# Optimization experiments

Hardware: AMD Instinct MI355X
Metric: run time of the kernel (lower is better)

## Reference

```python
import jax, jax.numpy as jnp
import numpy as np

NEG_SLOPE = 0.2  # PyG GATConv default leaky_relu slope

N_NODES = 50000
N_EDGES = 800000
IN_DIM = 128
HID = 32
HEADS = 4


def setup_inputs() -> dict:
    key = jax.random.key(0)
    ks = jax.random.split(key, 12)
    x = jax.random.normal(ks[0], (N_NODES, IN_DIM), dtype=jnp.float32)
    edge_index = jax.random.randint(ks[1], (2, N_EDGES), 0, N_NODES, dtype=jnp.int64)
    s1 = 1.0 / np.sqrt(IN_DIM)
    s2 = 1.0 / np.sqrt(HID * HEADS)
    return {
        "x": x,
        "edge_index": edge_index,
        # layer 1: GATConv(IN_DIM -> HID, heads=HEADS, concat=True)
        "W1": jax.random.normal(ks[2], (IN_DIM, HEADS * HID), dtype=jnp.float32) * s1,
        "a_src1": jax.random.normal(ks[3], (HEADS, HID), dtype=jnp.float32) * s1,
        "a_dst1": jax.random.normal(ks[4], (HEADS, HID), dtype=jnp.float32) * s1,
        "b1": jnp.zeros((HEADS * HID,), dtype=jnp.float32),
        # head: GATConv(HEADS*HID -> 1, heads=1, concat=False)
        "W2": jax.random.normal(ks[5], (HEADS * HID, 1), dtype=jnp.float32) * s2,
        "a_src2": jax.random.normal(ks[6], (1, 1), dtype=jnp.float32) * s2,
        "a_dst2": jax.random.normal(ks[7], (1, 1), dtype=jnp.float32) * s2,
        "b2": jnp.zeros((1,), dtype=jnp.float32),
    }


def gat_conv(x, src, dst, W, a_src, a_dst, b, heads, out_ch, concat, n_nodes):
    # linear transform -> [N, H, C]
    h = (x @ W).reshape(n_nodes, heads, out_ch)
    # per-node attention halves -> [N, H]
    alpha_s = jnp.einsum('nhc,hc->nh', h, a_src)
    alpha_d = jnp.einsum('nhc,hc->nh', h, a_dst)
    # per-edge logits (gather), leaky relu -> [E, H]
    e = jax.nn.leaky_relu(alpha_s[src] + alpha_d[dst], NEG_SLOPE)
    # segment softmax over destination neighborhoods
    m = jax.ops.segment_max(e, dst, num_segments=n_nodes)  # [N, H]
    m = jnp.where(jnp.isfinite(m), m, 0.0)
    ex = jnp.exp(e - m[dst])
    denom = jax.ops.segment_sum(ex, dst, num_segments=n_nodes)  # [N, H]
    alpha = ex / (denom[dst] + 1e-16)  # [E, H]
    # weighted scatter-aggregate of source messages
    msg = h[src] * alpha[:, :, None]  # [E, H, C]
    out = jax.ops.segment_sum(msg, dst, num_segments=n_nodes)  # [N, H, C]
    out = out.reshape(n_nodes, heads * out_ch) if concat else out.mean(axis=1)
    return out + b


def reference(x, edge_index, W1, a_src1, a_dst1, b1, W2, a_src2, a_dst2, b2):
    n = x.shape[0]
    # PyG GATConv adds self-loops by default
    loops = jnp.arange(n, dtype=edge_index.dtype)
    src = jnp.concatenate([edge_index[0], loops])
    dst = jnp.concatenate([edge_index[1], loops])
    h = gat_conv(x, src, dst, W1, a_src1, a_dst1, b1, HEADS, HID, True, n)
    h = jax.nn.elu(h)  # dropout inactive in eval mode
    out = gat_conv(h, src, dst, W2, a_src2, a_dst2, b2, 1, 1, False, n)
    return out.squeeze(-1)  # [N]
```

## Files before the change

kernel.cpp:

```cpp
#include <hip/hip_runtime.h>
#include <hip/hip_bf16.h>
#include <hip/hip_fp16.h>

#define N_NODES 50000
#define N_EDGES 800000
#define E_TOT   850000
#define GBLK 32
#define GEMM_BLOCKS 1563
#define NR 196
#define EPB 4096
#define BIN_BLOCKS 208
#define WT_BLOCKS 32
#define SEGCAP 8192

typedef _Float16 half8 __attribute__((ext_vector_type(8)));
typedef float f32x16 __attribute__((ext_vector_type(16)));

__global__ __launch_bounds__(512) void bin_kernel(const int* __restrict__ ei,
                                                  int* __restrict__ rangeCursor,
                                                  unsigned* __restrict__ gseg,
                                                  const float* __restrict__ W1,
                                                  _Float16* __restrict__ Wt) {
    __shared__ int cnt[NR];
    __shared__ int gbase[NR];
    const int tid = threadIdx.x;

    if (blockIdx.x >= BIN_BLOCKS) {
        int k = (blockIdx.x - BIN_BLOCKS) * 4 + (tid >> 7);
        int c = tid & 127;
        Wt[c * 128 + k] = (_Float16)W1[k * 128 + c];
        return;
    }

    for (int i = tid; i < NR; i += 512) cnt[i] = 0;
    __syncthreads();

    int e0 = blockIdx.x * EPB + tid * 8;
    bool valid = (e0 < E_TOT);
    int src[8], dst[8], rg[8], rk[8];
    if (valid) {
        if (e0 < N_EDGES) {
            int4 a = *(const int4*)(ei + e0);
            int4 b = *(const int4*)(ei + e0 + 4);
            int4 c = *(const int4*)(ei + N_EDGES + e0);
            int4 d = *(const int4*)(ei + N_EDGES + e0 + 4);
            src[0]=a.x; src[1]=a.y; src[2]=a.z; src[3]=a.w;
            src[4]=b.x; src[5]=b.y; src[6]=b.z; src[7]=b.w;
            dst[0]=c.x; dst[1]=c.y; dst[2]=c.z; dst[3]=c.w;
            dst[4]=d.x; dst[5]=d.y; dst[6]=d.z; dst[7]=d.w;
        } else {
#pragma unroll
            for (int k = 0; k < 8; k++) { src[k] = dst[k] = e0 + k - N_EDGES; }
        }
#pragma unroll
        for (int k = 0; k < 8; k++) {
            rg[k] = dst[k] >> 8;
            rk[k] = atomicAdd(&cnt[rg[k]], 1);
        }
    }
    __syncthreads();
    for (int i = tid; i < NR; i += 512) {
        int c = cnt[i];
        gbase[i] = c ? atomicAdd(&rangeCursor[i], c) : 0;
    }
    __syncthreads();
    if (valid) {
#pragma unroll
        for (int k = 0; k < 8; k++) {
            int pos = gbase[rg[k]] + rk[k];
            if (pos < SEGCAP)
                gseg[(size_t)rg[k] * SEGCAP + pos] =
                    ((unsigned)(dst[k] & 255) << 17) | (unsigned)src[k];
        }
    }
}

__global__ __launch_bounds__(512) void fatgf_kernel(const int* __restrict__ rangeCursor,
                                                    const unsigned* __restrict__ gseg,
                                                    int* __restrict__ offs,
                                                    int* __restrict__ bucket,
                                                    const float* __restrict__ x,
                                                    const _Float16* __restrict__ Wt,
                                                    const float* __restrict__ asrc1,
                                                    const float* __restrict__ adst1,
                                                    __half* __restrict__ h1,
                                                    float* __restrict__ as1,
                                                    float* __restrict__ ad1) {
    __shared__ __align__(16) char smem[(1024 + SEGCAP) * 4];
    const int tid = threadIdx.x;

    if (blockIdx.x < NR) {
        int* rsc  = (int*)smem;
        int* cnt  = rsc + 256;
        int* csc  = cnt + 256;
        int* cur  = csc + 256;
        int* lbuf = cur + 256;
        const int r = blockIdx.x;

        if (tid < 256) rsc[tid] = (tid < NR) ? min(rangeCursor[tid], SEGCAP) : 0;
        __syncthreads();
        for (int d = 1; d < 256; d <<= 1) {
            int u = (tid < 256 && tid >= d) ? rsc[tid - d] : 0;
            __syncthreads();
            if (tid < 256) rsc[tid] += u;
            __syncthreads();
        }
        const int n = min(rangeCursor[r], SEGCAP);
        const int rbase = rsc[r] - n;
        const unsigned* __restrict__ seg = gseg + (size_t)r * SEGCAP;

        if (tid < 256) cnt[tid] = 0;
        __syncthreads();
        for (int i = tid; i < n; i += 512)
            atomicAdd(&cnt[seg[i] >> 17], 1);
        __syncthreads();
        if (tid < 256) csc[tid] = cnt[tid];
        __syncthreads();
        for (int d = 1; d < 256; d <<= 1) {
            int u = (tid < 256 && tid >= d) ? csc[tid - d] : 0;
            __syncthreads();
            if (tid < 256) csc[tid] += u;
            __syncthreads();
        }
        if (tid < 256) {
            int lofs = csc[tid] - cnt[tid];
            cur[tid] = lofs;
            int node = r * 256 + tid;
            if (node < N_NODES) offs[node] = rbase + lofs;
        }
        if (r == NR - 1 && tid == 0) offs[N_NODES] = rbase + n;
        __syncthreads();
        for (int i = tid; i < n; i += 512) {
            unsigned en = seg[i];
            int p = atomicAdd(&cur[en >> 17], 1);
            lbuf[p] = (int)(en & 0x1FFFFu);
        }
        __syncthreads();
        for (int i = tid; i < n; i += 512)
            bucket[rbase + i] = lbuf[i];
        return;
    }

    if (tid >= 256) return;

    _Float16* hl = (_Float16*)smem;
    const int l    = tid & 63;
    const int w    = tid >> 6;
    const int g    = l >> 5;
    const int cl   = l & 31;
    const int col  = 32 * w + cl;
    const int base = (blockIdx.x - NR) * GBLK;
    int r = base + cl;
    int rc = (r < N_NODES) ? r : 0;

    const half8* wt8 = (const half8*)(Wt + col * 128);
    half8 bf0 = wt8[0 + g], bf1 = wt8[2 + g], bf2 = wt8[4 + g], bf3 = wt8[6 + g];
    half8 bf4 = wt8[8 + g], bf5 = wt8[10 + g], bf6 = wt8[12 + g], bf7 = wt8[14 + g];

    const float* xr = x + (size_t)rc * 128 + 8 * g;
    f32x16 acc = {};
#define GAT_MFMA_STEP(S, BF)                                                  \
    {                                                                         \
        float4 u0 = *(const float4*)(xr + 16 * S);                            \
        float4 u1 = *(const float4*)(xr + 16 * S + 4);                        \
        half8 af;                                                             \
        af[0] = (_Float16)u0.x; af[1] = (_Float16)u0.y;                       \
        af[2] = (_Float16)u0.z; af[3] = (_Float16)u0.w;                       \
        af[4] = (_Float16)u1.x; af[5] = (_Float16)u1.y;                       \
        af[6] = (_Float16)u1.z; af[7] = (_Float16)u1.w;                       \
        acc = __builtin_amdgcn_mfma_f32_32x32x16_f16(af, BF, acc, 0, 0, 0);   \
    }
    GAT_MFMA_STEP(0, bf0) GAT_MFMA_STEP(1, bf1) GAT_MFMA_STEP(2, bf2)
    GAT_MFMA_STEP(3, bf3) GAT_MFMA_STEP(4, bf4) GAT_MFMA_STEP(5, bf5)
    GAT_MFMA_STEP(6, bf6) GAT_MFMA_STEP(7, bf7)
#undef GAT_MFMA_STEP

#pragma unroll
    for (int j = 0; j < 16; j++) {
        int nl = (j & 3) + 8 * (j >> 2) + 4 * g;
        hl[nl * 136 + col] = (_Float16)acc[j];
    }
    __syncthreads();

    {
        int nl = tid >> 3, c8 = tid & 7;
        int node = base + nl;
        if (node < N_NODES) {
            float4 v0 = *(const float4*)(hl + nl * 136 + c8 * 16);
            float4 v1 = *(const float4*)(hl + nl * 136 + c8 * 16 + 8);
            float4* dst = (float4*)(h1 + (size_t)node * 128 + c8 * 16);
            dst[0] = v0;
            dst[1] = v1;
        }
    }
    {
        int nh = tid >> 1, which = tid & 1;
        int nl = nh & 31, head = nh >> 5;
        int node = base + nl;
        if (node < N_NODES) {
            const float* av = (which ? adst1 : asrc1) + head * 32;
            const _Float16* hp = hl + nl * 136 + head * 32;
            float s = 0.f;
#pragma unroll
            for (int j = 0; j < 32; j++)
                s += (float)hp[j] * av[j];
            (which ? ad1 : as1)[node * 4 + head] = s;
        }
    }
}

__global__ __launch_bounds__(256) void agg1_kernel(const __half* __restrict__ h1,
                                                   const float* __restrict__ as1,
                                                   const float* __restrict__ ad1,
                                                   const int* __restrict__ offs,
                                                   const int* __restrict__ bucket,
                                                   const float* __restrict__ b1,
                                                   const float* __restrict__ W2,
                                                   float* __restrict__ h2s) {
    __shared__ int   sbuf[4][64];
    __shared__ float exbuf[4][64][4];

    int w = threadIdx.x >> 6, l = threadIdx.x & 63;
    int node = blockIdx.x * 4 + w;
    if (node >= N_NODES) return;
    int sub = l & 15;
    int ep  = l >> 4;
    int head = sub >> 2;
    int a = offs[node];
    int deg = offs[node + 1] - a;
    float4 adv = *(const float4*)(ad1 + (size_t)node * 4);

    float c[8];
#pragma unroll
    for (int k = 0; k < 8; k++) c[k] = 0.f;
    float sx = 0.f;

    for (int base = 0; base < deg; base += 64) {
        int cd = min(deg - base, 64);
        {
            bool v = l < cd;
            int s = bucket[a + base + (v ? l : 0)];
            sbuf[w][l] = s;
            float4 asv = *(const float4*)(as1 + (size_t)s * 4);
            float e0 = asv.x + adv.x, e1 = asv.y + adv.y;
            float e2 = asv.z + adv.z, e3 = asv.w + adv.w;
            e0 = fmaxf(e0, 0.2f * e0);
            e1 = fmaxf(e1, 0.2f * e1);
            e2 = fmaxf(e2, 0.2f * e2);
            e3 = fmaxf(e3, 0.2f * e3);
            float4 exv;
            exv.x = v ? __expf(e0) : 0.f;
            exv.y = v ? __expf(e1) : 0.f;
            exv.z = v ? __expf(e2) : 0.f;
            exv.w = v ? __expf(e3) : 0.f;
            *(float4*)&exbuf[w][l][0] = exv;
        }
        __builtin_amdgcn_wave_barrier();
        for (int g = 0; g < cd; g += 4) {
            int j = g + ep;
            bool v2 = j < cd;
            int jj = v2 ? j : 0;
            int s = sbuf[w][jj];
            float ex = exbuf[w][jj][head];
            if (!v2) ex = 0.f;
            float4 hv = *(const float4*)(h1 + (size_t)s * 128 + sub * 8);
            const __half2* hh = (const __half2*)&hv;
            float2 f0 = __half22float2(hh[0]);
            float2 f1 = __half22float2(hh[1]);
            float2 f2 = __half22float2(hh[2]);
            float2 f3 = __half22float2(hh[3]);
            sx += ex;
            c[0] += ex * f0.x; c[1] += ex * f0.y;
            c[2] += ex * f1.x; c[3] += ex * f1.y;
            c[4] += ex * f2.x; c[5] += ex * f2.y;
            c[6] += ex * f3.x; c[7] += ex * f3.y;
        }
        __builtin_amdgcn_wave_barrier();
    }

#pragma unroll
    for (int k = 0; k < 8; k++) {
        c[k] += __shfl_xor(c[k], 16, 64);
        c[k] += __shfl_xor(c[k], 32, 64);
    }
    sx += __shfl_xor(sx, 16, 64);
    sx += __shfl_xor(sx, 32, 64);

    float r = 1.f / (sx + 1e-16f);
    float4 blo = ((const float4*)b1)[sub * 2];
    float4 bhi = ((const float4*)b1)[sub * 2 + 1];
    float4 wlo = ((const float4*)W2)[sub * 2];
    float4 whi = ((const float4*)W2)[sub * 2 + 1];
    float ob[8] = {blo.x, blo.y, blo.z, blo.w, bhi.x, bhi.y, bhi.z, bhi.w};
    float ow[8] = {wlo.x, wlo.y, wlo.z, wlo.w, whi.x, whi.y, whi.z, whi.w};
    float p = 0.f;
#pragma unroll
    for (int k = 0; k < 8; k++) {
        float o = c[k] * r + ob[k];
        float el = (o > 0.f) ? o : (__expf(o) - 1.f);
        p += el * ow[k];
    }
    p += __shfl_xor(p, 1, 64);
    p += __shfl_xor(p, 2, 64);
    p += __shfl_xor(p, 4, 64);
    p += __shfl_xor(p, 8, 64);
    if (l == 0) h2s[node] = p;
}

__global__ __launch_bounds__(256) void agg2_kernel(const float* __restrict__ h2s,
                                                   const int* __restrict__ offs,
                                                   const int* __restrict__ bucket,
                                                   const float* __restrict__ asrc2,
                                                   const float* __restrict__ adst2,
                                                   const float* __restrict__ b2,
                                                   float* __restrict__ out) {
    int w = threadIdx.x >> 6, l = threadIdx.x & 63;
    int node = blockIdx.x * 4 + w;
    if (node >= N_NODES) return;
    float asc = asrc2[0], adc = adst2[0], bias = b2[0];
    float adn = h2s[node] * adc;
    int a = offs[node], b = offs[node + 1];
    float sx = 0.f, sw = 0.f;
    for (int i = a + l; i < b; i += 64) {
        float hs = h2s[bucket[i]];
        float e = hs * asc + adn;
        e = fmaxf(e, 0.2f * e);
        float ex = __expf(e);
        sx += ex;
        sw += ex * hs;
    }
#pragma unroll
    for (int o = 32; o > 0; o >>= 1) {
        sx += __shfl_xor(sx, o, 64);
        sw += __shfl_xor(sw, o, 64);
    }
    if (l == 0) out[node] = sw / (sx + 1e-16f) + bias;
}


extern "C" void kernel_launch(void* const* d_in, const int* in_sizes, int n_in,
                              void* d_out, int out_size, void* d_ws, size_t ws_size,
                              hipStream_t stream) {
    const float* x     = (const float*)d_in[0];
    const int*   ei    = (const int*)d_in[1];
    const float* W1    = (const float*)d_in[2];
    const float* asrc1 = (const float*)d_in[3];
    const float* adst1 = (const float*)d_in[4];
    const float* b1    = (const float*)d_in[5];
    const float* W2    = (const float*)d_in[6];
    const float* asrc2 = (const float*)d_in[7];
    const float* adst2 = (const float*)d_in[8];
    const float* b2    = (const float*)d_in[9];
    float* out = (float*)d_out;

    char* ws = (char*)d_ws;
    size_t o = 0;
    auto alloc = [&](size_t bytes) -> void* {
        void* p = ws + o;
        o += (bytes + 255) & ~(size_t)255;
        return p;
    };
    int* offs    = (int*)alloc((size_t)(N_NODES + 1) * 4);
    int* bucket  = (int*)alloc((size_t)E_TOT * 4);
    __half* h1   = (__half*)alloc((size_t)N_NODES * 128 * 2);
    float* as1   = (float*)alloc((size_t)N_NODES * 4 * 4);
    float* ad1   = (float*)alloc((size_t)N_NODES * 4 * 4);
    float* h2s   = (float*)alloc((size_t)N_NODES * 4);
    int* rangeCursor = (int*)alloc((size_t)NR * 4);
    unsigned* gseg   = (unsigned*)alloc((size_t)NR * SEGCAP * 4);
    _Float16* Wt     = (_Float16*)alloc((size_t)128 * 128 * 2);

    hipMemsetAsync(rangeCursor, 0, (size_t)NR * 4, stream);

    bin_kernel<<<BIN_BLOCKS + WT_BLOCKS, 512, 0, stream>>>(ei, rangeCursor, gseg, W1, Wt);

    fatgf_kernel<<<NR + GEMM_BLOCKS, 512, 0, stream>>>(
        rangeCursor, gseg, offs, bucket,
        x, Wt, asrc1, adst1, h1, as1, ad1);

    agg1_kernel<<<(N_NODES + 3) / 4, 256, 0, stream>>>(
        h1, as1, ad1, offs, bucket, b1, W2, h2s);

    agg2_kernel<<<(N_NODES + 3) / 4, 256, 0, stream>>>(
        h2s, offs, bucket, asrc2, adst2, b2, out);
}
```

Before: 95.21 us.

## Stage x tile in LDS as fp16 and double GEMM rows per block

The node-feature GEMM block now handles 64 rows instead of 32 and uses all 512 threads instead of idling half of them. The x tile is loaded with coalesced float4 reads, converted to fp16 once, and stored in a padded LDS buffer; each MFMA wave then reads its A operand from LDS. The attention-score epilogue is remapped to the 64-row tile. This aims to improve global load coalescing and cut block count and per-block overhead, at the cost of more LDS per block and an extra barrier.

Measured after the change: 110.5 us. +16.1%, slower.

```diff
diff --git a/kernel.cpp b/kernel.cpp
--- a/kernel.cpp
+++ b/kernel.cpp
@@ -5,13 +5,14 @@
 #define N_NODES 50000
 #define N_EDGES 800000
 #define E_TOT   850000
-#define GBLK 32
-#define GEMM_BLOCKS 1563
+#define GBLK 64
+#define GEMM_BLOCKS 782
 #define NR 196
 #define EPB 4096
 #define BIN_BLOCKS 208
 #define WT_BLOCKS 32
 #define SEGCAP 8192
+#define XS_STRIDE 134
 
 typedef _Float16 half8 __attribute__((ext_vector_type(8)));
 typedef float f32x16 __attribute__((ext_vector_type(16)));
@@ -141,44 +142,54 @@
         return;
     }
 
-    if (tid >= 256) return;
-
-    _Float16* hl = (_Float16*)smem;
-    const int l    = tid & 63;
-    const int w    = tid >> 6;
-    const int g    = l >> 5;
-    const int cl   = l & 31;
-    const int col  = 32 * w + cl;
+    _Float16* xs = (_Float16*)smem;
+    _Float16* hl = (_Float16*)(smem + 64 * XS_STRIDE * 2);
     const int base = (blockIdx.x - NR) * GBLK;
-    int r = base + cl;
-    int rc = (r < N_NODES) ? r : 0;
-
-    const half8* wt8 = (const half8*)(Wt + col * 128);
-    half8 bf0 = wt8[0 + g], bf1 = wt8[2 + g], bf2 = wt8[4 + g], bf3 = wt8[6 + g];
-    half8 bf4 = wt8[8 + g], bf5 = wt8[10 + g], bf6 = wt8[12 + g], bf7 = wt8[14 + g];
-
-    const float* xr = x + (size_t)rc * 128 + 8 * g;
-    f32x16 acc = {};
-#define GAT_MFMA_STEP(S, BF)                                                  \
-    {                                                                         \
-        float4 u0 = *(const float4*)(xr + 16 * S);                            \
-        float4 u1 = *(const float4*)(xr + 16 * S + 4);                        \
-        half8 af;                                                             \
-        af[0] = (_Float16)u0.x; af[1] = (_Float16)u0.y;                       \
-        af[2] = (_Float16)u0.z; af[3] = (_Float16)u0.w;                       \
-        af[4] = (_Float16)u1.x; af[5] = (_Float16)u1.y;                       \
-        af[6] = (_Float16)u1.z; af[7] = (_Float16)u1.w;                       \
-        acc = __builtin_amdgcn_mfma_f32_32x32x16_f16(af, BF, acc, 0, 0, 0);   \
-    }
-    GAT_MFMA_STEP(0, bf0) GAT_MFMA_STEP(1, bf1) GAT_MFMA_STEP(2, bf2)
-    GAT_MFMA_STEP(3, bf3) GAT_MFMA_STEP(4, bf4) GAT_MFMA_STEP(5, bf5)
-    GAT_MFMA_STEP(6, bf6) GAT_MFMA_STEP(7, bf7)
+
+#pragma unroll
+    for (int it = 0; it < 4; it++) {
+        int idx = tid + it * 512;
+        int row = idx >> 5, c4 = idx & 31;
+        int n2 = base + row;
+        float4 v = make_float4(0.f, 0.f, 0.f, 0.f);
+        if (n2 < N_NODES)
+            v = *(const float4*)(x + (size_t)n2 * 128 + c4 * 4);
+        _Float16 h4[4] = {(_Float16)v.x, (_Float16)v.y, (_Float16)v.z, (_Float16)v.w};
+        *(double*)(xs + row * XS_STRIDE + c4 * 4) = *(double*)h4;
+    }
+    __syncthreads();
+
+    {
+        const int l    = tid & 63;
+        const int w    = tid >> 6;
+        const int g    = l >> 5;
+        const int cl   = l & 31;
+        const int ct   = w & 3;
+        const int R0   = (w >> 2) * 32;
+        const int col  = 32 * ct + cl;
+
+        const half8* wt8 = (const half8*)(Wt + col * 128);
+        half8 bf0 = wt8[0 + g], bf1 = wt8[2 + g], bf2 = wt8[4 + g], bf3 = wt8[6 + g];
+        half8 bf4 = wt8[8 + g], bf5 = wt8[10 + g], bf6 = wt8[12 + g], bf7 = wt8[14 + g];
+
+        const _Float16* xr = xs + (R0 + cl) * XS_STRIDE + 8 * g;
+        f32x16 acc = {};
+#define GAT_MFMA_STEP(S, BF)                                                   \
+        {                                                                      \
+            half8 af = *(const half8*)(xr + 16 * S);                           \
+            acc = __builtin_amdgcn_mfma_f32_32x32x16_f16(af, BF, acc, 0, 0, 0); \
+        }
+        GAT_MFMA_STEP(0, bf0) GAT_MFMA_STEP(1, bf1) GAT_MFMA_STEP(2, bf2)
+        GAT_MFMA_STEP(3, bf3) GAT_MFMA_STEP(4, bf4) GAT_MFMA_STEP(5, bf5)
+        GAT_MFMA_STEP(6, bf6) GAT_MFMA_STEP(7, bf7)
 #undef GAT_MFMA_STEP
 
-#pragma unroll
-    for (int j = 0; j < 16; j++) {
-        int nl = (j & 3) + 8 * (j >> 2) + 4 * g;
-        hl[nl * 136 + col] = (_Float16)acc[j];
+        __syncthreads();
+#pragma unroll
+        for (int j = 0; j < 16; j++) {
+            int nl = R0 + (j & 3) + 8 * (j >> 2) + 4 * g;
+            hl[nl * 136 + col] = (_Float16)acc[j];
+        }
     }
     __syncthreads();
 
@@ -194,8 +205,8 @@
         }
     }
     {
-        int nh = tid >> 1, which = tid & 1;
-        int nl = nh & 31, head = nh >> 5;
+        int which = tid & 1, nh = tid >> 1;
+        int nl = nh & 63, head = nh >> 6;
         int node = base + nl;
         if (node < N_NODES) {
             const float* av = (which ? adst1 : asrc1) + head * 32;
```
